# Kernel tuning notes

Hardware: AMD Instinct MI355X
Metric: run time of the kernel (lower is better)

## Reference

```python
import jax, jax.numpy as jnp
import numpy as np

N = 4096       # num_nodes (must equal out_features: final div broadcasts [C,N]/[N,1])
IN_F = 1024    # module in_features
OUT_F = 4096   # module out_features == N
F_RAW = 512    # raw node feature dim fed to the in-forward Linear


def setup_inputs() -> dict:
    key = jax.random.key(0)
    ks = jax.random.split(key, 5)
    node_features = jax.random.normal(ks[0], (N, F_RAW), dtype=jnp.float32)
    adjacency_matrix = jax.random.bernoulli(ks[1], 0.004, (N, N)).astype(jnp.float32)
    eye = jnp.eye(N, dtype=jnp.float32)
    A0 = adjacency_matrix * (1.0 - eye)                 # adjacency w/o self loops
    S = (A0 @ A0 + A0) * (1.0 - eye)                    # sibling matrix, zero diag
    mask_hadamard = S[:, None, :]                       # [N,1,N]
    mask_father = adjacency_matrix[:, None, :]          # [N,1,N]
    neighbor_count = jnp.maximum(A0.sum(axis=1, keepdims=True), 1.0)  # [N,1]
    lim = float(1.0 / np.sqrt(F_RAW))
    linear_w = jax.random.uniform(ks[2], (IN_F, F_RAW), minval=-lim, maxval=lim, dtype=jnp.float32)
    linear_b = jax.random.uniform(ks[3], (IN_F,), minval=-lim, maxval=lim, dtype=jnp.float32)
    weight = jax.random.normal(ks[4], (IN_F, OUT_F), dtype=jnp.float32) * float(np.sqrt(2.0 / IN_F))
    return dict(node_features=node_features, adjacency_matrix=adjacency_matrix,
                mask_father=mask_father, neighbor_count=neighbor_count,
                mask_hadamard=mask_hadamard, linear_w=linear_w, linear_b=linear_b,
                weight=weight)


def reference(node_features, adjacency_matrix, mask_father, neighbor_count,
              mask_hadamard, linear_w, linear_b, weight):
    # Linear + projection: wf[n,c]
    x = node_features @ linear_w.T + linear_b           # [N, IN_F]
    wf = x @ weight                                      # [N, C]
    # Original builds masked_hadamard[j,i,c] = wf[i,c]*wf[j,c]*S[i,j] ([N,C,N]),
    # contracts with adjacency over i, masks with adj[k,j], sums over k:
    #   sum_hadamard[c,j] = wf[j,c] * sum_i (sum_k adj[k,j]*adj[k,i]) * S[i,j] * wf[i,c]
    # Fused form avoids the O(N^2 C) intermediates; same math.
    A_out = mask_father[:, 0, :]                         # adj[k,j]  [N,N]
    S = mask_hadamard[:, 0, :]                           # S[i,j]    [N,N]
    G = A_out.T @ adjacency_matrix                       # G[j,i] = sum_k adj[k,j]*adj[k,i]
    P = G * S.T                                          # P[j,i] = G[j,i]*S[i,j]
    sum_hadamard = (wf * (P @ wf)).T                     # [C, N]
    # Final broadcast division exactly as torch: [C,N] / [N,1] (requires C==N)
    return sum_hadamard / jnp.square(neighbor_count)
```

## Files before the change

### kernel.cpp

```cpp
#include <hip/hip_runtime.h>
#include <hip/hip_bf16.h>

typedef __attribute__((ext_vector_type(8))) short s16x8;
typedef __attribute__((ext_vector_type(4))) float f32x4;
typedef __attribute__((ext_vector_type(8))) unsigned short u16x8;

__device__ __forceinline__ float b2f(unsigned short u) {
  union { unsigned int i; float f; } x; x.i = ((unsigned int)u) << 16; return x.f;
}
__device__ __forceinline__ unsigned short f2b(float f) {
  __hip_bfloat16 h = __float2bfloat16(f);
  return *reinterpret_cast<unsigned short*>(&h);
}

#define TILE 128
#define BK 32
#define PCAP 128
#define SCAP 1024

template <int EPI>
__device__ __forceinline__ void gemm_body(
    unsigned short* As, unsigned short* Bs,
    int bx, int by,
    const unsigned short* __restrict__ A,
    const unsigned short* __restrict__ B,
    unsigned short* __restrict__ C,
    int M, int N, int K,
    const float* __restrict__ epi_f)
{
  const int tid  = threadIdx.x;
  const int lane = tid & 63;
  const int wave = tid >> 6;
  const int wm = (wave & 1) * 64;
  const int wn = (wave >> 1) * 64;
  const long bm = (long)by * TILE;
  const long bn = (long)bx * TILE;

  f32x4 acc[4][4] = {};

  auto STAGE = [&](int kt, int b) {
    const long kb = (long)kt * BK;
#pragma unroll
    for (int i = 0; i < 2; ++i) {
      const int c0 = (wave * 2 + i) * 64;
      const int c  = c0 + lane;
      const int r  = c >> 2;
      const int cc = ((c & 3) ^ ((c >> 3) & 3)) * 8;
      const unsigned short* ga = A + (bm + r) * (long)K + kb + cc;
      const unsigned short* gb = B + (bn + r) * (long)K + kb + cc;
      __builtin_amdgcn_global_load_lds(
          (const __attribute__((address_space(1))) void*)ga,
          (__attribute__((address_space(3))) void*)(As + b * (TILE * BK) + c0 * 8), 16, 0, 0);
      __builtin_amdgcn_global_load_lds(
          (const __attribute__((address_space(1))) void*)gb,
          (__attribute__((address_space(3))) void*)(Bs + b * (TILE * BK) + c0 * 8), 16, 0, 0);
    }
  };

  const int kTiles = K / BK;
  STAGE(0, 0);

  for (int kt = 0; kt < kTiles; ++kt) {
    const int cur = kt & 1;
    if (kt + 1 < kTiles) {
      STAGE(kt + 1, cur ^ 1);
      asm volatile("s_waitcnt vmcnt(4)" ::: "memory");
    } else {
      asm volatile("s_waitcnt vmcnt(0)" ::: "memory");
    }
    __builtin_amdgcn_sched_barrier(0);
    __builtin_amdgcn_s_barrier();
    __builtin_amdgcn_sched_barrier(0);

    const int rl = lane & 15;
    const int kqx = ((lane >> 4) ^ ((rl >> 1) & 3)) * 8;
    s16x8 af[4], bfr[4];
#pragma unroll
    for (int mi = 0; mi < 4; ++mi)
      af[mi] = *(const s16x8*)(As + cur * (TILE * BK) + (wm + mi * 16 + rl) * BK + kqx);
#pragma unroll
    for (int ni = 0; ni < 4; ++ni)
      bfr[ni] = *(const s16x8*)(Bs + cur * (TILE * BK) + (wn + ni * 16 + rl) * BK + kqx);
#pragma unroll
    for (int mi = 0; mi < 4; ++mi)
#pragma unroll
      for (int ni = 0; ni < 4; ++ni)
        acc[mi][ni] = __builtin_amdgcn_mfma_f32_16x16x32_bf16(af[mi], bfr[ni], acc[mi][ni], 0, 0, 0);

    __builtin_amdgcn_sched_barrier(0);
    __builtin_amdgcn_s_barrier();
    __builtin_amdgcn_sched_barrier(0);
  }

  const int cl = lane & 15;
  const int rq = (lane >> 4) * 4;
#pragma unroll
  for (int mi = 0; mi < 4; ++mi)
#pragma unroll
    for (int ni = 0; ni < 4; ++ni)
#pragma unroll
      for (int r = 0; r < 4; ++r) {
        const long row = bm + wm + mi * 16 + rq + r;
        const long col = bn + wn + ni * 16 + cl;
        float v = acc[mi][ni][r];
        if (EPI == 1) v += epi_f[col];
        C[row * (long)N + col] = f2b(v);
      }
}

__device__ __forceinline__ void colbits_body(
    int i, const float* __restrict__ adj, unsigned long long* __restrict__ colb)
{
  const int t = threadIdx.x;
  const unsigned long long bit = 1ull << (i & 63);
  const int w = i >> 6;
  const float* r = adj + (long)i * 4096;
#pragma unroll
  for (int q = 0; q < 4; ++q) {
    int c = (t + q * 256) * 4;
    float4 v = *(const float4*)(r + c);
    if (v.x != 0.f) atomicOr(&colb[(long)(c + 0) * 64 + w], bit);
    if (v.y != 0.f) atomicOr(&colb[(long)(c + 1) * 64 + w], bit);
    if (v.z != 0.f) atomicOr(&colb[(long)(c + 2) * 64 + w], bit);
    if (v.w != 0.f) atomicOr(&colb[(long)(c + 3) * 64 + w], bit);
  }
}

__device__ __forceinline__ void p2_body(
    char* smem, int k,
    const float* __restrict__ S, const unsigned long long* __restrict__ colb,
    int* __restrict__ pk, float* __restrict__ pv, int* __restrict__ pcnt)
{
  unsigned long long* ck = (unsigned long long*)smem;
  int*   jl = (int*)(smem + 512);
  float* sl = (float*)(smem + 512 + SCAP * 4);
  int*   msh = (int*)(smem + 512 + SCAP * 8);
  const int t = threadIdx.x;
  const int lane = t & 63;
  if (t == 0) *msh = 0;
  if (t < 64) ck[t] = colb[(long)k * 64 + t];
  __syncthreads();
  const float* Sr = S + (long)k * 4096;
  const unsigned long long lmask = (1ull << lane) - 1ull;
#pragma unroll
  for (int q = 0; q < 4; ++q) {
    int c = (t + q * 256) * 4;
    float4 v = *(const float4*)(Sr + c);
    float vals[4] = { v.x, v.y, v.z, v.w };
#pragma unroll
    for (int r = 0; r < 4; ++r) {
      float vv = vals[r];
      unsigned long long mask = __ballot(vv != 0.f);
      if (mask) {
        int base;
        if (lane == 0) base = atomicAdd(msh, __popcll(mask));
        base = __shfl(base, 0, 64);
        if (vv != 0.f) {
          int pos = base + __popcll(mask & lmask);
          if (pos < SCAP) { jl[pos] = c + r; sl[pos] = vv; }
        }
      }
    }
  }
  __syncthreads();
  const int mm = min(*msh, SCAP);
  const int l = t & 7;
  for (int idx = (t >> 3); idx < mm; idx += 32) {
    const int j = jl[idx];
    const ulonglong2* cj = (const ulonglong2*)(colb + (long)j * 64);
    int cnt = 0;
#pragma unroll
    for (int it = 0; it < 4; ++it) {
      ulonglong2 q  = cj[it * 8 + l];
      ulonglong2 cc = *(const ulonglong2*)&ck[it * 16 + l * 2];
      cnt += __popcll(q.x & cc.x) + __popcll(q.y & cc.y);
    }
    cnt += __shfl_down(cnt, 4, 8);
    cnt += __shfl_down(cnt, 2, 8);
    cnt += __shfl_down(cnt, 1, 8);
    if (l == 0 && cnt > 0) {
      int slot = atomicAdd(&pcnt[j], 1);
      if (slot < PCAP) {
        pk[(long)j * PCAP + slot] = k;
        pv[(long)j * PCAP + slot] = (float)cnt * sl[idx];
      }
    }
  }
}

__global__ __launch_bounds__(256) void prep_fused(
    const float* __restrict__ w,  unsigned short* __restrict__ weightT,
    const float* __restrict__ nf, unsigned short* __restrict__ nfb,
    const float* __restrict__ lw, unsigned short* __restrict__ lwb,
    float* __restrict__ zp)
{
  __shared__ unsigned short tile[64][66];
  const int b = blockIdx.x;
  const int t = threadIdx.x;
  if (b < 1024) {
    const int R = 1024, C = 4096;
    const long r0 = (long)(b >> 6) * 64;
    const long c0 = (long)(b & 63) * 64;
#pragma unroll
    for (int i = 0; i < 4; ++i) {
      int v = t + i * 256;
      int r = v >> 4;
      int c = (v & 15) * 4;
      float4 d = *(const float4*)(w + (r0 + r) * (long)C + c0 + c);
      tile[r][c + 0] = f2b(d.x); tile[r][c + 1] = f2b(d.y);
      tile[r][c + 2] = f2b(d.z); tile[r][c + 3] = f2b(d.w);
    }
    __syncthreads();
#pragma unroll
    for (int i = 0; i < 4; ++i) {
      int v = t + i * 256;
      int r = v >> 4;
      int c = (v & 15) * 4;
      ushort4 d;
      d.x = tile[c + 0][r]; d.y = tile[c + 1][r]; d.z = tile[c + 2][r]; d.w = tile[c + 3][r];
      *(ushort4*)(weightT + (c0 + r) * (long)R + r0 + c) = d;
    }
  } else if (b < 3072) {
    const long e = ((long)(b - 1024) * 256 + t) * 4;
    float4 d = *(const float4*)(nf + e);
    ushort4 o;
    o.x = f2b(d.x); o.y = f2b(d.y); o.z = f2b(d.z); o.w = f2b(d.w);
    *(ushort4*)(nfb + e) = o;
  } else if (b < 3584) {
    const long e = ((long)(b - 3072) * 256 + t) * 4;
    float4 d = *(const float4*)(lw + e);
    ushort4 o;
    o.x = f2b(d.x); o.y = f2b(d.y); o.z = f2b(d.z); o.w = f2b(d.w);
    *(ushort4*)(lwb + e) = o;
  } else {
    const long e = ((long)(b - 3584) * 256 + t) * 4;
    *(float4*)(zp + e) = make_float4(0.f, 0.f, 0.f, 0.f);
  }
}

__global__ __launch_bounds__(256) void g1_colbits(
    const unsigned short* __restrict__ nfb, const unsigned short* __restrict__ lwb,
    unsigned short* __restrict__ x, const float* __restrict__ lb,
    const float* __restrict__ adj, unsigned long long* __restrict__ colb)
{
  extern __shared__ ulonglong2 dsm[];
  const int b = blockIdx.x;
  if (b < 256) {
    unsigned short* As = (unsigned short*)dsm;
    unsigned short* Bs = As + 2 * TILE * BK;
    gemm_body<1>(As, Bs, b & 7, b >> 3, nfb, lwb, x, 4096, 1024, 512, lb);
  } else {
    colbits_body(b - 256, adj, colb);
  }
}

__global__ __launch_bounds__(256) void g0_p2(
    const unsigned short* __restrict__ x, const unsigned short* __restrict__ weightT,
    unsigned short* __restrict__ wf,
    const float* __restrict__ S, const unsigned long long* __restrict__ colb,
    int* __restrict__ pk, float* __restrict__ pv, int* __restrict__ pcnt)
{
  extern __shared__ ulonglong2 dsm[];
  const int b = blockIdx.x;
  if (b % 5 == 0) {
    const int g = b / 5;
    unsigned short* As = (unsigned short*)dsm;
    unsigned short* Bs = As + 2 * TILE * BK;
    gemm_body<0>(As, Bs, g & 31, g >> 5, x, weightT, wf, 4096, 4096, 1024, nullptr);
  } else {
    const int k = b - b / 5 - 1;
    p2_body((char*)dsm, k, S, colb, pk, pv, pcnt);
  }
}

__global__ __launch_bounds__(256) void spmm_fused(
    const int* __restrict__ pk, const float* __restrict__ pv,
    const int* __restrict__ pcnt, const unsigned short* __restrict__ wf,
    const float* __restrict__ nc, float* __restrict__ VO)
{
  __shared__ int   k_l[4][PCAP];
  __shared__ float v_l[4][PCAP];
  __shared__ int   n_s[4];
  const int t = threadIdx.x;
  const int wave = t >> 6;
  const int lane = t & 63;
  const int seg = blockIdx.x;
  const int jb  = blockIdx.y * 4;
  {
    int e0 = t;
    k_l[e0 >> 7][e0 & 127] = pk[(long)(jb + (e0 >> 7)) * PCAP + (e0 & 127)];
    v_l[e0 >> 7][e0 & 127] = pv[(long)(jb + (e0 >> 7)) * PCAP + (e0 & 127)];
    int e1 = t + 256;
    k_l[e1 >> 7][e1 & 127] = pk[(long)(jb + (e1 >> 7)) * PCAP + (e1 & 127)];
    v_l[e1 >> 7][e1 & 127] = pv[(long)(jb + (e1 >> 7)) * PCAP + (e1 & 127)];
    if (t < 4) n_s[t] = min(pcnt[jb + t], PCAP);
  }
  __syncthreads();
  const int j = jb + wave;
  const int n = n_s[wave];
  const int* __restrict__ kk = k_l[wave];
  const float* __restrict__ vv = v_l[wave];
  const int c0 = seg * 512 + lane * 8;

  float acc[8] = {};
  int m = 0;
  for (; m + 8 <= n; m += 8) {
    float vs[8];
    u16x8 d[8];
#pragma unroll
    for (int r = 0; r < 8; ++r) {
      vs[r] = vv[m + r];
      d[r] = *(const u16x8*)(wf + (unsigned)(kk[m + r] * 4096 + c0));
    }
    __builtin_amdgcn_sched_barrier(0);
#pragma unroll
    for (int r = 0; r < 8; ++r)
#pragma unroll
      for (int q = 0; q < 8; ++q)
        acc[q] += vs[r] * b2f(d[r][q]);
  }
  for (; m + 2 <= n; m += 2) {
    const float v0 = vv[m], v1 = vv[m + 1];
    u16x8 a = *(const u16x8*)(wf + (unsigned)(kk[m]     * 4096 + c0));
    u16x8 b = *(const u16x8*)(wf + (unsigned)(kk[m + 1] * 4096 + c0));
#pragma unroll
    for (int q = 0; q < 8; ++q) acc[q] += v0 * b2f(a[q]) + v1 * b2f(b[q]);
  }
  for (; m < n; ++m) {
    const float va = vv[m];
    u16x8 a = *(const u16x8*)(wf + (unsigned)(kk[m] * 4096 + c0));
#pragma unroll
    for (int q = 0; q < 8; ++q) acc[q] += va * b2f(a[q]);
  }
  u16x8 wa = *(const u16x8*)(wf + (unsigned)(j * 4096 + c0));
  float out[8];
#pragma unroll
  for (int q = 0; q < 8; q += 4) {
    float4 nv = *(const float4*)(nc + c0 + q);
    float n4[4] = { nv.x, nv.y, nv.z, nv.w };
#pragma unroll
    for (int r = 0; r < 4; ++r)
      out[q + r] = acc[q + r] * b2f(wa[q + r]) / (n4[r] * n4[r]);
  }
  float* dst = VO + (long)j * 4096 + c0;
  *(float4*)(dst + 0) = make_float4(out[0], out[1], out[2], out[3]);
  *(float4*)(dst + 4) = make_float4(out[4], out[5], out[6], out[7]);
}

__global__ __launch_bounds__(256) void final_transpose(float* __restrict__ D)
{
  const int bx = blockIdx.x, by = blockIdx.y;
  if (by > bx) return;
  const int X = bx * 64, Y = by * 64;
  const bool diag = (bx == by);
  __shared__ float t1[64][65];
  __shared__ float t2[64][65];
  const int t = threadIdx.x;
  const int r0 = t >> 4;
  const int c4 = (t & 15) * 4;
#pragma unroll
  for (int i = 0; i < 4; ++i) {
    int r = r0 + i * 16;
    float4 d = *(const float4*)&D[(long)(Y + r) * 4096 + X + c4];
    t1[r][c4 + 0] = d.x; t1[r][c4 + 1] = d.y; t1[r][c4 + 2] = d.z; t1[r][c4 + 3] = d.w;
    if (!diag) {
      float4 e = *(const float4*)&D[(long)(X + r) * 4096 + Y + c4];
      t2[r][c4 + 0] = e.x; t2[r][c4 + 1] = e.y; t2[r][c4 + 2] = e.z; t2[r][c4 + 3] = e.w;
    }
  }
  __syncthreads();
#pragma unroll
  for (int i = 0; i < 4; ++i) {
    int r = r0 + i * 16;
    float4 o;
    o.x = t1[c4 + 0][r]; o.y = t1[c4 + 1][r]; o.z = t1[c4 + 2][r]; o.w = t1[c4 + 3][r];
    *(float4*)&D[(long)(X + r) * 4096 + Y + c4] = o;
    if (!diag) {
      float4 p;
      p.x = t2[c4 + 0][r]; p.y = t2[c4 + 1][r]; p.z = t2[c4 + 2][r]; p.w = t2[c4 + 3][r];
      *(float4*)&D[(long)(Y + r) * 4096 + X + c4] = p;
    }
  }
}

extern "C" void kernel_launch(void* const* d_in, const int* in_sizes, int n_in,
                              void* d_out, int out_size, void* d_ws, size_t ws_size,
                              hipStream_t stream) {
  const float* nf  = (const float*)d_in[0];
  const float* adj = (const float*)d_in[1];
  const float* nc  = (const float*)d_in[3];
  const float* S   = (const float*)d_in[4];
  const float* lw  = (const float*)d_in[5];
  const float* lb  = (const float*)d_in[6];
  const float* w   = (const float*)d_in[7];

  char* ws = (char*)d_ws;
  unsigned short*      wf      = (unsigned short*)(ws);
  unsigned long long*  colb    = (unsigned long long*)(ws + (32ll << 20));
  int*                 pcnt    = (int*)(ws + (34ll << 20));
  int*                 pk      = (int*)(ws + (35ll << 20));
  float*               pv      = (float*)(ws + (37ll << 20));
  unsigned short*      weightT = (unsigned short*)(ws + (40ll << 20));
  unsigned short*      nfb     = (unsigned short*)(ws + (48ll << 20));
  unsigned short*      lwb     = (unsigned short*)(ws + (52ll << 20));
  unsigned short*      x       = (unsigned short*)(ws + (54ll << 20));
  float*               VO      = (float*)d_out;

  prep_fused<<<4100, 256, 0, stream>>>(w, weightT, nf, nfb, lw, lwb, (float*)colb);
  g1_colbits<<<4352, 256, 32768, stream>>>(nfb, lwb, x, lb, adj, colb);
  g0_p2<<<5120, 256, 32768, stream>>>(x, weightT, wf, S, colb, pk, pv, pcnt);
  spmm_fused<<<dim3(8, 1024), 256, 0, stream>>>(pk, pv, pcnt, wf, nc, VO);
  final_transpose<<<dim3(64, 64), 256, 0, stream>>>(VO);
}
```

Before: 382.1 us.

## Replace double-buffered GEMM LDS staging with single buffer and plain syncthreads

Drops the two-stage LDS ping-pong in the shared bf16 GEMM body. Each k-tile is now loaded into a single buffer, followed by a __syncthreads, the MFMA work, and another __syncthreads. This halves the dynamic LDS per block (32 KB to 16 KB), which could allow more resident blocks, but it gives up overlapping the next tile's global-to-LDS loads with the current tile's MFMAs. The fused p2 and colbits paths share the same dynamic LDS allocation and must still fit in the smaller size.

After: 398.1 us. 1.04x slower.

```diff
diff --git a/kernel.cpp b/kernel.cpp
--- a/kernel.cpp
+++ b/kernel.cpp
@@ -38,7 +38,8 @@
 
   f32x4 acc[4][4] = {};
 
-  auto STAGE = [&](int kt, int b) {
+  const int kTiles = K / BK;
+  for (int kt = 0; kt < kTiles; ++kt) {
     const long kb = (long)kt * BK;
 #pragma unroll
     for (int i = 0; i < 2; ++i) {
@@ -50,46 +51,28 @@
       const unsigned short* gb = B + (bn + r) * (long)K + kb + cc;
       __builtin_amdgcn_global_load_lds(
           (const __attribute__((address_space(1))) void*)ga,
-          (__attribute__((address_space(3))) void*)(As + b * (TILE * BK) + c0 * 8), 16, 0, 0);
+          (__attribute__((address_space(3))) void*)(As + c0 * 8), 16, 0, 0);
       __builtin_amdgcn_global_load_lds(
           (const __attribute__((address_space(1))) void*)gb,
-          (__attribute__((address_space(3))) void*)(Bs + b * (TILE * BK) + c0 * 8), 16, 0, 0);
-    }
-  };
-
-  const int kTiles = K / BK;
-  STAGE(0, 0);
-
-  for (int kt = 0; kt < kTiles; ++kt) {
-    const int cur = kt & 1;
-    if (kt + 1 < kTiles) {
-      STAGE(kt + 1, cur ^ 1);
-      asm volatile("s_waitcnt vmcnt(4)" ::: "memory");
-    } else {
-      asm volatile("s_waitcnt vmcnt(0)" ::: "memory");
-    }
-    __builtin_amdgcn_sched_barrier(0);
-    __builtin_amdgcn_s_barrier();
-    __builtin_amdgcn_sched_barrier(0);
+          (__attribute__((address_space(3))) void*)(Bs + c0 * 8), 16, 0, 0);
+    }
+    __syncthreads();
 
     const int rl = lane & 15;
     const int kqx = ((lane >> 4) ^ ((rl >> 1) & 3)) * 8;
     s16x8 af[4], bfr[4];
 #pragma unroll
     for (int mi = 0; mi < 4; ++mi)
-      af[mi] = *(const s16x8*)(As + cur * (TILE * BK) + (wm + mi * 16 + rl) * BK + kqx);
+      af[mi] = *(const s16x8*)(As + (wm + mi * 16 + rl) * BK + kqx);
 #pragma unroll
     for (int ni = 0; ni < 4; ++ni)
-      bfr[ni] = *(const s16x8*)(Bs + cur * (TILE * BK) + (wn + ni * 16 + rl) * BK + kqx);
+      bfr[ni] = *(const s16x8*)(Bs + (wn + ni * 16 + rl) * BK + kqx);
 #pragma unroll
     for (int mi = 0; mi < 4; ++mi)
 #pragma unroll
       for (int ni = 0; ni < 4; ++ni)
         acc[mi][ni] = __builtin_amdgcn_mfma_f32_16x16x32_bf16(af[mi], bfr[ni], acc[mi][ni], 0, 0, 0);
-
-    __builtin_amdgcn_sched_barrier(0);
-    __builtin_amdgcn_s_barrier();
-    __builtin_amdgcn_sched_barrier(0);
+    __syncthreads();
   }
 
   const int cl = lane & 15;
@@ -247,7 +230,7 @@
   const int b = blockIdx.x;
   if (b < 256) {
     unsigned short* As = (unsigned short*)dsm;
-    unsigned short* Bs = As + 2 * TILE * BK;
+    unsigned short* Bs = As + TILE * BK;
     gemm_body<1>(As, Bs, b & 7, b >> 3, nfb, lwb, x, 4096, 1024, 512, lb);
   } else {
     colbits_body(b - 256, adj, colb);
@@ -265,7 +248,7 @@
   if (b % 5 == 0) {
     const int g = b / 5;
     unsigned short* As = (unsigned short*)dsm;
-    unsigned short* Bs = As + 2 * TILE * BK;
+    unsigned short* Bs = As + TILE * BK;
     gemm_body<0>(As, Bs, g & 31, g >> 5, x, weightT, wf, 4096, 4096, 1024, nullptr);
   } else {
     const int k = b - b / 5 - 1;
@@ -407,8 +390,8 @@
   float*               VO      = (float*)d_out;
 
   prep_fused<<<4100, 256, 0, stream>>>(w, weightT, nf, nfb, lw, lwb, (float*)colb);
-  g1_colbits<<<4352, 256, 32768, stream>>>(nfb, lwb, x, lb, adj, colb);
-  g0_p2<<<5120, 256, 32768, stream>>>(x, weightT, wf, S, colb, pk, pv, pcnt);
+  g1_colbits<<<4352, 256, 16384, stream>>>(nfb, lwb, x, lb, adj, colb);
+  g0_p2<<<5120, 256, 16384, stream>>>(x, weightT, wf, S, colb, pk, pv, pcnt);
   spmm_fused<<<dim3(8, 1024), 256, 0, stream>>>(pk, pv, pcnt, wf, nc, VO);
   final_transpose<<<dim3(64, 64), 256, 0, stream>>>(VO);
 }
```
